# Performance work log

Hardware: AMD Instinct MI355X
Metric: run time of the kernel (lower is better)

The kernel has to match this reference:

```python
import jax, jax.numpy as jnp
import numpy as np

B, S, C, H = 1024, 254, 2, 1024
TIME_DIM = 64
HALF = TIME_DIM // 2
N_STEPS = 50


def time_embed(t):
    # t: [B] -> [B, 64] sinusoidal embedding, matching SinusoidalEmbedding(64)
    freqs = jnp.exp(jnp.arange(HALF, dtype=jnp.float32) * (-np.log(10000.0) / (HALF - 1)))
    ang = t[:, None] * freqs[None, :]  # [B, 32]
    return jnp.concatenate([jnp.sin(ang), jnp.cos(ang)], axis=-1)  # [B, 64]


def setup_inputs() -> dict:
    key = jax.random.key(0)
    ks = jax.random.split(key, 12)
    inp = {}
    inp["state"] = jax.random.normal(ks[0], (B, S), jnp.float32)
    inp["x0"] = jax.random.normal(ks[1], (B, C), jnp.float32)  # initial noise of sample()
    dims = [S + C + TIME_DIM, H, H, H, H, C]  # 320 -> 1024 x4 -> 2
    for i in range(5):
        kw, kb = jax.random.split(ks[2 + i])
        inp[f"W{i}"] = jax.random.normal(kw, (dims[i], dims[i + 1]), jnp.float32) * (1.0 / np.sqrt(dims[i]))
        inp[f"b{i}"] = jax.random.normal(kb, (dims[i + 1],), jnp.float32) * 0.01
    return inp


def reference(state, x0, W0, b0, W1, b1, W2, b2, W3, b3, W4, b4):
    dt = 1.0 / N_STEPS

    def velocity(x, t):
        temb = time_embed(t)
        h = jnp.concatenate([state, x, temb], axis=-1)  # [B, 320]
        h = jax.nn.silu(h @ W0 + b0)
        h = jax.nn.silu(h @ W1 + b1)
        h = jax.nn.silu(h @ W2 + b2)
        h = jax.nn.silu(h @ W3 + b3)
        return h @ W4 + b4  # [B, C]

    def step(x, i):
        t = jnp.full((state.shape[0],), i * dt, dtype=jnp.float32)
        return x + dt * velocity(x, t), None

    x, _ = jax.lax.scan(step, x0, jnp.arange(N_STEPS, dtype=jnp.float32))
    return x
```

## Files before the change

### kernel.cpp

```cpp
#include <hip/hip_runtime.h>


typedef __bf16 bf16x8 __attribute__((ext_vector_type(8)));
typedef float  f32x4  __attribute__((ext_vector_type(4)));
typedef unsigned short u16;
typedef u16 u16x8 __attribute__((ext_vector_type(8)));
typedef u16 u16x4 __attribute__((ext_vector_type(4)));

#define H 1024
#define BATCH 1024
#define SDIM 254
#define NSTEP 50
#define DT 0.02f
#define LDP 40

__device__ __forceinline__ u16 f2bf(float f) {
  unsigned int u = __float_as_uint(f);
  return (u16)((u + 0x7FFFu + ((u >> 16) & 1u)) >> 16);
}

__device__ __forceinline__ float silu(float v) {
  return v / (1.0f + __expf(-v));
}

__global__ void transpose_w(const float* __restrict__ A, const float* __restrict__ B,
                            const float* __restrict__ C, u16* __restrict__ TA,
                            u16* __restrict__ TB, u16* __restrict__ TC) {
  const float* W = (blockIdx.z == 0) ? A : (blockIdx.z == 1) ? B : C;
  u16* T = (blockIdx.z == 0) ? TA : (blockIdx.z == 1) ? TB : TC;
  __shared__ float tile[32][33];
  const int n0 = blockIdx.x * 32, k0 = blockIdx.y * 32;
  const int tx = threadIdx.x & 31, ty = threadIdx.x >> 5;
#pragma unroll
  for (int i = 0; i < 4; ++i)
    tile[ty + 8 * i][tx] = W[(k0 + ty + 8 * i) * H + n0 + tx];
  __syncthreads();
#pragma unroll
  for (int i = 0; i < 4; ++i)
    T[(size_t)(n0 + ty + 8 * i) * H + k0 + tx] = f2bf(tile[tx][ty + 8 * i]);
}

__global__ void base_gemm(const float* __restrict__ state, const float* __restrict__ W0,
                          const float* __restrict__ b0, float* __restrict__ base) {
  __shared__ float srow[SDIM];
  const int b = blockIdx.x, tid = threadIdx.x;
  if (tid < SDIM) srow[tid] = state[b * SDIM + tid];
  __syncthreads();
  const int n = tid * 4;
  float4 bv = *(const float4*)&b0[n];
  float a0 = bv.x, a1 = bv.y, a2 = bv.z, a3 = bv.w;
  for (int k = 0; k < SDIM; ++k) {
    float s = srow[k];
    float4 w = *(const float4*)&W0[k * H + n];
    a0 += s * w.x; a1 += s * w.y; a2 += s * w.z; a3 += s * w.w;
  }
  float4 r = {a0, a1, a2, a3};
  *(float4*)&base[(size_t)b * H + n] = r;
}

__global__ void tvec_kernel(const float* __restrict__ W0, float* __restrict__ tvec) {
  const int s = blockIdx.x;
  const int h = blockIdx.y * 256 + threadIdx.x;
  const float t = (float)s * DT;
  float acc = 0.0f;
#pragma unroll
  for (int j = 0; j < 32; ++j) {
    float fr = __expf((float)j * (-9.210340371976184f / 31.0f));
    float ang = t * fr;
    acc += __sinf(ang) * W0[(256 + j) * H + h] + __cosf(ang) * W0[(288 + j) * H + h];
  }
  tvec[s * H + h] = acc;
}

__global__ void init_kernel(const float* __restrict__ base, const float* __restrict__ tvec,
                            const float* __restrict__ x0, const float* __restrict__ W0,
                            u16* __restrict__ h0, float* __restrict__ xout) {
  const int b = blockIdx.x, tid = threadIdx.x;
  const float xa = x0[2 * b], xb = x0[2 * b + 1];
  if (tid == 0) { xout[2 * b] = xa; xout[2 * b + 1] = xb; }
  const int n = tid * 4;
  float4 bs = *(const float4*)&base[(size_t)b * H + n];
  float4 tv = *(const float4*)&tvec[n];
  float4 wa = *(const float4*)&W0[254 * H + n];
  float4 wb = *(const float4*)&W0[255 * H + n];
  u16x4 r;
  r[0] = f2bf(silu(bs.x + tv.x + xa * wa.x + xb * wb.x));
  r[1] = f2bf(silu(bs.y + tv.y + xa * wa.y + xb * wb.y));
  r[2] = f2bf(silu(bs.z + tv.z + xa * wa.z + xb * wb.z));
  r[3] = f2bf(silu(bs.w + tv.w + xa * wa.w + xb * wb.w));
  *(u16x4*)&h0[(size_t)b * H + n] = r;
}

__global__ __launch_bounds__(64) void gemm_mfma(const u16* __restrict__ A,
                                                const u16* __restrict__ BT,
                                                const float* __restrict__ bias,
                                                void* __restrict__ out, int out_bf16) {
  __shared__ u16 As[32 * LDP];
  __shared__ u16 Bs[32 * LDP];
  const int tid = threadIdx.x;
  const int bn = blockIdx.x, bm = blockIdx.y;
  const int lr = tid & 15, quad = tid >> 4;

  const int srow = tid >> 2;
  const int skc = (tid & 3) * 8;

  const u16* Ap = A + (size_t)(bm * 32 + srow) * H + skc;
  const u16* Bp = BT + (size_t)(bn * 32 + srow) * H + skc;

  f32x4 acc[2][2] = {};

  u16x8 ga0 = *(const u16x8*)(Ap);
  u16x8 ga1 = *(const u16x8*)(Ap + 16 * H);
  u16x8 gb0 = *(const u16x8*)(Bp);
  u16x8 gb1 = *(const u16x8*)(Bp + 16 * H);

  for (int kt = 0; kt < 32; ++kt) {
    *(u16x8*)&As[srow * LDP + skc] = ga0;
    *(u16x8*)&As[(srow + 16) * LDP + skc] = ga1;
    *(u16x8*)&Bs[srow * LDP + skc] = gb0;
    *(u16x8*)&Bs[(srow + 16) * LDP + skc] = gb1;
    if (kt < 31) {
      const int off = (kt + 1) * 32;
      ga0 = *(const u16x8*)(Ap + off);
      ga1 = *(const u16x8*)(Ap + 16 * H + off);
      gb0 = *(const u16x8*)(Bp + off);
      gb1 = *(const u16x8*)(Bp + 16 * H + off);
    }
    bf16x8 a0 = *(const bf16x8*)&As[lr * LDP + quad * 8];
    bf16x8 a1 = *(const bf16x8*)&As[(16 + lr) * LDP + quad * 8];
    bf16x8 b0 = *(const bf16x8*)&Bs[lr * LDP + quad * 8];
    bf16x8 b1 = *(const bf16x8*)&Bs[(16 + lr) * LDP + quad * 8];
    acc[0][0] = __builtin_amdgcn_mfma_f32_16x16x32_bf16(a0, b0, acc[0][0], 0, 0, 0);
    acc[0][1] = __builtin_amdgcn_mfma_f32_16x16x32_bf16(a0, b1, acc[0][1], 0, 0, 0);
    acc[1][0] = __builtin_amdgcn_mfma_f32_16x16x32_bf16(a1, b0, acc[1][0], 0, 0, 0);
    acc[1][1] = __builtin_amdgcn_mfma_f32_16x16x32_bf16(a1, b1, acc[1][1], 0, 0, 0);
  }

#pragma unroll
  for (int mt = 0; mt < 2; ++mt)
#pragma unroll
    for (int nt = 0; nt < 2; ++nt) {
      const int gm = bm * 32 + mt * 16 + quad * 4;
      const int gn = bn * 32 + nt * 16 + lr;
      const float bv = bias[gn];
      f32x4 v = acc[mt][nt];
#pragma unroll
      for (int r = 0; r < 4; ++r) {
        float x = silu(v[r] + bv);
        if (out_bf16) ((u16*)out)[(size_t)(gm + r) * H + gn] = f2bf(x);
        else          ((float*)out)[(size_t)(gm + r) * H + gn] = x;
      }
    }
}

__global__ void tail_kernel(const float* __restrict__ h3, const float* __restrict__ W4,
                            const float* __restrict__ b4, float* __restrict__ x,
                            const float* __restrict__ base, const float* __restrict__ tvec,
                            const float* __restrict__ W0, u16* __restrict__ h0, int s) {
  const int b = blockIdx.x, tid = threadIdx.x;
  float s0 = 0.0f, s1 = 0.0f;
  for (int h = tid; h < H; h += 256) {
    float v = h3[(size_t)b * H + h];
    s0 += v * W4[2 * h];
    s1 += v * W4[2 * h + 1];
  }
#pragma unroll
  for (int o = 32; o > 0; o >>= 1) {
    s0 += __shfl_down(s0, o);
    s1 += __shfl_down(s1, o);
  }
  __shared__ float red[8];
  __shared__ float xs[2];
  const int w = tid >> 6;
  if ((tid & 63) == 0) { red[w * 2] = s0; red[w * 2 + 1] = s1; }
  __syncthreads();
  if (tid == 0) {
    float v0 = red[0] + red[2] + red[4] + red[6] + b4[0];
    float v1 = red[1] + red[3] + red[5] + red[7] + b4[1];
    float xa = x[2 * b] + DT * v0;
    float xb = x[2 * b + 1] + DT * v1;
    x[2 * b] = xa; x[2 * b + 1] = xb;
    xs[0] = xa; xs[1] = xb;
  }
  __syncthreads();
  if (s < NSTEP - 1) {
    const float xa = xs[0], xb = xs[1];
    const int n = tid * 4;
    float4 bs = *(const float4*)&base[(size_t)b * H + n];
    float4 tv = *(const float4*)&tvec[(size_t)(s + 1) * H + n];
    float4 wa = *(const float4*)&W0[254 * H + n];
    float4 wb = *(const float4*)&W0[255 * H + n];
    u16x4 r;
    r[0] = f2bf(silu(bs.x + tv.x + xa * wa.x + xb * wb.x));
    r[1] = f2bf(silu(bs.y + tv.y + xa * wa.y + xb * wb.y));
    r[2] = f2bf(silu(bs.z + tv.z + xa * wa.z + xb * wb.z));
    r[3] = f2bf(silu(bs.w + tv.w + xa * wa.w + xb * wb.w));
    *(u16x4*)&h0[(size_t)b * H + n] = r;
  }
}

extern "C" void kernel_launch(void* const* d_in, const int* in_sizes, int n_in,
                              void* d_out, int out_size, void* d_ws, size_t ws_size,
                              hipStream_t stream) {
  const float* state = (const float*)d_in[0];
  const float* x0    = (const float*)d_in[1];
  const float* W0    = (const float*)d_in[2];
  const float* b0    = (const float*)d_in[3];
  const float* W1    = (const float*)d_in[4];
  const float* b1    = (const float*)d_in[5];
  const float* W2    = (const float*)d_in[6];
  const float* b2    = (const float*)d_in[7];
  const float* W3    = (const float*)d_in[8];
  const float* b3    = (const float*)d_in[9];
  const float* W4    = (const float*)d_in[10];
  const float* b4    = (const float*)d_in[11];
  float* xout = (float*)d_out;

  char* ws = (char*)d_ws;
  const size_t MB = 1024 * 1024;
  float* base = (float*)(ws + 0);
  float* h3f  = (float*)(ws + 4 * MB);
  float* tvec = (float*)(ws + 8 * MB);
  u16* w1t = (u16*)(ws + 8 * MB + 256 * 1024);
  u16* w2t = (u16*)(ws + 10 * MB + 256 * 1024);
  u16* w3t = (u16*)(ws + 12 * MB + 256 * 1024);
  u16* hA  = (u16*)(ws + 14 * MB + 256 * 1024);
  u16* hB  = (u16*)(ws + 16 * MB + 256 * 1024);
  u16* hC  = (u16*)(ws + 18 * MB + 256 * 1024);

  transpose_w<<<dim3(32, 32, 3), 256, 0, stream>>>(W1, W2, W3, w1t, w2t, w3t);
  base_gemm<<<BATCH, 256, 0, stream>>>(state, W0, b0, base);
  tvec_kernel<<<dim3(NSTEP, 4), 256, 0, stream>>>(W0, tvec);
  init_kernel<<<BATCH, 256, 0, stream>>>(base, tvec, x0, W0, hA, xout);

  for (int s = 0; s < NSTEP; ++s) {
    gemm_mfma<<<dim3(32, 32), 64, 0, stream>>>(hA, w1t, b1, hB, 1);
    gemm_mfma<<<dim3(32, 32), 64, 0, stream>>>(hB, w2t, b2, hC, 1);
    gemm_mfma<<<dim3(32, 32), 64, 0, stream>>>(hC, w3t, b3, h3f, 0);
    tail_kernel<<<BATCH, 256, 0, stream>>>(h3f, W4, b4, xout, base, tvec, W0, hA, s);
  }
}
```

Baseline: 1.837 ms.

## Load MFMA operands directly from global with 8-deep register prefetch, swizzle tiles

The GEMM kernel drops the shared-memory staging and loads bf16x8 fragments straight from global memory into registers, keeping eight k-tiles in flight as a rotating prefetch buffer. Block indices are remapped so groups of 8 M-tiles share an N-tile, which should improve L2 reuse. The fp32 state x W0 base GEMM is replaced by a bf16 transpose of W0, a bf16 padded copy of state, and the templated MFMA kernel. This removes LDS round-trips and barriers per k-step, at the cost of more registers and bf16 precision in the base projection.

```diff
diff --git a/kernel.cpp b/kernel.cpp
--- a/kernel.cpp
+++ b/kernel.cpp
@@ -4,7 +4,6 @@
 typedef __bf16 bf16x8 __attribute__((ext_vector_type(8)));
 typedef float  f32x4  __attribute__((ext_vector_type(4)));
 typedef unsigned short u16;
-typedef u16 u16x8 __attribute__((ext_vector_type(8)));
 typedef u16 u16x4 __attribute__((ext_vector_type(4)));
 
 #define H 1024
@@ -12,7 +11,6 @@
 #define SDIM 254
 #define NSTEP 50
 #define DT 0.02f
-#define LDP 40
 
 __device__ __forceinline__ u16 f2bf(float f) {
   unsigned int u = __float_as_uint(f);
@@ -40,22 +38,22 @@
     T[(size_t)(n0 + ty + 8 * i) * H + k0 + tx] = f2bf(tile[tx][ty + 8 * i]);
 }
 
-__global__ void base_gemm(const float* __restrict__ state, const float* __restrict__ W0,
-                          const float* __restrict__ b0, float* __restrict__ base) {
-  __shared__ float srow[SDIM];
-  const int b = blockIdx.x, tid = threadIdx.x;
-  if (tid < SDIM) srow[tid] = state[b * SDIM + tid];
-  __syncthreads();
-  const int n = tid * 4;
-  float4 bv = *(const float4*)&b0[n];
-  float a0 = bv.x, a1 = bv.y, a2 = bv.z, a3 = bv.w;
-  for (int k = 0; k < SDIM; ++k) {
-    float s = srow[k];
-    float4 w = *(const float4*)&W0[k * H + n];
-    a0 += s * w.x; a1 += s * w.y; a2 += s * w.z; a3 += s * w.w;
-  }
-  float4 r = {a0, a1, a2, a3};
-  *(float4*)&base[(size_t)b * H + n] = r;
+__global__ void transpose_w0(const float* __restrict__ W0, u16* __restrict__ T) {
+  __shared__ float tile[32][33];
+  const int n0 = blockIdx.x * 32, k0 = blockIdx.y * 32;
+  const int tx = threadIdx.x & 31, ty = threadIdx.x >> 5;
+#pragma unroll
+  for (int i = 0; i < 4; ++i)
+    tile[ty + 8 * i][tx] = W0[(k0 + ty + 8 * i) * H + n0 + tx];
+  __syncthreads();
+#pragma unroll
+  for (int i = 0; i < 4; ++i)
+    T[(size_t)(n0 + ty + 8 * i) * 256 + k0 + tx] = f2bf(tile[tx][ty + 8 * i]);
+}
+
+__global__ void prep_state(const float* __restrict__ state, u16* __restrict__ sb) {
+  const int row = blockIdx.x, col = threadIdx.x;
+  sb[row * 256 + col] = (col < SDIM) ? f2bf(state[row * SDIM + col]) : (u16)0;
 }
 
 __global__ void tvec_kernel(const float* __restrict__ W0, float* __restrict__ tvec) {
@@ -91,49 +89,45 @@
   *(u16x4*)&h0[(size_t)b * H + n] = r;
 }
 
+template <int KTILES, int MODE>
 __global__ __launch_bounds__(64) void gemm_mfma(const u16* __restrict__ A,
                                                 const u16* __restrict__ BT,
                                                 const float* __restrict__ bias,
-                                                void* __restrict__ out, int out_bf16) {
-  __shared__ u16 As[32 * LDP];
-  __shared__ u16 Bs[32 * LDP];
+                                                void* __restrict__ out) {
   const int tid = threadIdx.x;
-  const int bn = blockIdx.x, bm = blockIdx.y;
   const int lr = tid & 15, quad = tid >> 4;
-
-  const int srow = tid >> 2;
-  const int skc = (tid & 3) * 8;
-
-  const u16* Ap = A + (size_t)(bm * 32 + srow) * H + skc;
-  const u16* Bp = BT + (size_t)(bn * 32 + srow) * H + skc;
-
+  const int lin = blockIdx.x + 32 * blockIdx.y;
+  const int bm = (lin & 7) | ((lin >> 8) << 3);
+  const int bn = (lin >> 3) & 31;
+  const int K = KTILES * 32;
+
+  const bf16x8* Ap0 = (const bf16x8*)(A + (size_t)(bm * 32 + lr) * K + quad * 8);
+  const bf16x8* Ap1 = (const bf16x8*)(A + (size_t)(bm * 32 + 16 + lr) * K + quad * 8);
+  const bf16x8* Bp0 = (const bf16x8*)(BT + (size_t)(bn * 32 + lr) * K + quad * 8);
+  const bf16x8* Bp1 = (const bf16x8*)(BT + (size_t)(bn * 32 + 16 + lr) * K + quad * 8);
   f32x4 acc[2][2] = {};
-
-  u16x8 ga0 = *(const u16x8*)(Ap);
-  u16x8 ga1 = *(const u16x8*)(Ap + 16 * H);
-  u16x8 gb0 = *(const u16x8*)(Bp);
-  u16x8 gb1 = *(const u16x8*)(Bp + 16 * H);
-
-  for (int kt = 0; kt < 32; ++kt) {
-    *(u16x8*)&As[srow * LDP + skc] = ga0;
-    *(u16x8*)&As[(srow + 16) * LDP + skc] = ga1;
-    *(u16x8*)&Bs[srow * LDP + skc] = gb0;
-    *(u16x8*)&Bs[(srow + 16) * LDP + skc] = gb1;
-    if (kt < 31) {
-      const int off = (kt + 1) * 32;
-      ga0 = *(const u16x8*)(Ap + off);
-      ga1 = *(const u16x8*)(Ap + 16 * H + off);
-      gb0 = *(const u16x8*)(Bp + off);
-      gb1 = *(const u16x8*)(Bp + 16 * H + off);
+  bf16x8 pa0[8], pa1[8], pb0[8], pb1[8];
+#pragma unroll
+  for (int d = 0; d < 8 && d < KTILES; ++d) {
+    pa0[d] = Ap0[d * 4];
+    pa1[d] = Ap1[d * 4];
+    pb0[d] = Bp0[d * 4];
+    pb1[d] = Bp1[d * 4];
+  }
+#pragma unroll
+  for (int kt = 0; kt < KTILES; ++kt) {
+    const int s = kt & 7;
+    acc[0][0] = __builtin_amdgcn_mfma_f32_16x16x32_bf16(pa0[s], pb0[s], acc[0][0], 0, 0, 0);
+    acc[0][1] = __builtin_amdgcn_mfma_f32_16x16x32_bf16(pa0[s], pb1[s], acc[0][1], 0, 0, 0);
+    acc[1][0] = __builtin_amdgcn_mfma_f32_16x16x32_bf16(pa1[s], pb0[s], acc[1][0], 0, 0, 0);
+    acc[1][1] = __builtin_amdgcn_mfma_f32_16x16x32_bf16(pa1[s], pb1[s], acc[1][1], 0, 0, 0);
+    if (kt + 8 < KTILES) {
+      const int off = (kt + 8) * 4;
+      pa0[s] = Ap0[off];
+      pa1[s] = Ap1[off];
+      pb0[s] = Bp0[off];
+      pb1[s] = Bp1[off];
     }
-    bf16x8 a0 = *(const bf16x8*)&As[lr * LDP + quad * 8];
-    bf16x8 a1 = *(const bf16x8*)&As[(16 + lr) * LDP + quad * 8];
-    bf16x8 b0 = *(const bf16x8*)&Bs[lr * LDP + quad * 8];
-    bf16x8 b1 = *(const bf16x8*)&Bs[(16 + lr) * LDP + quad * 8];
-    acc[0][0] = __builtin_amdgcn_mfma_f32_16x16x32_bf16(a0, b0, acc[0][0], 0, 0, 0);
-    acc[0][1] = __builtin_amdgcn_mfma_f32_16x16x32_bf16(a0, b1, acc[0][1], 0, 0, 0);
-    acc[1][0] = __builtin_amdgcn_mfma_f32_16x16x32_bf16(a1, b0, acc[1][0], 0, 0, 0);
-    acc[1][1] = __builtin_amdgcn_mfma_f32_16x16x32_bf16(a1, b1, acc[1][1], 0, 0, 0);
   }
 
 #pragma unroll
@@ -146,9 +140,10 @@
       f32x4 v = acc[mt][nt];
 #pragma unroll
       for (int r = 0; r < 4; ++r) {
-        float x = silu(v[r] + bv);
-        if (out_bf16) ((u16*)out)[(size_t)(gm + r) * H + gn] = f2bf(x);
-        else          ((float*)out)[(size_t)(gm + r) * H + gn] = x;
+        float x = v[r] + bv;
+        if (MODE != 2) x = silu(x);
+        if (MODE == 0) ((u16*)out)[(size_t)(gm + r) * H + gn] = f2bf(x);
+        else           ((float*)out)[(size_t)(gm + r) * H + gn] = x;
       }
     }
 }
@@ -227,16 +222,20 @@
   u16* hA  = (u16*)(ws + 14 * MB + 256 * 1024);
   u16* hB  = (u16*)(ws + 16 * MB + 256 * 1024);
   u16* hC  = (u16*)(ws + 18 * MB + 256 * 1024);
+  u16* w0t = (u16*)(ws + 20 * MB + 256 * 1024);
+  u16* stb = (u16*)(ws + 21 * MB);
 
   transpose_w<<<dim3(32, 32, 3), 256, 0, stream>>>(W1, W2, W3, w1t, w2t, w3t);
-  base_gemm<<<BATCH, 256, 0, stream>>>(state, W0, b0, base);
+  transpose_w0<<<dim3(32, 8), 256, 0, stream>>>(W0, w0t);
+  prep_state<<<BATCH, 256, 0, stream>>>(state, stb);
+  gemm_mfma<8, 2><<<dim3(32, 32), 64, 0, stream>>>(stb, w0t, b0, base);
   tvec_kernel<<<dim3(NSTEP, 4), 256, 0, stream>>>(W0, tvec);
   init_kernel<<<BATCH, 256, 0, stream>>>(base, tvec, x0, W0, hA, xout);
 
   for (int s = 0; s < NSTEP; ++s) {
-    gemm_mfma<<<dim3(32, 32), 64, 0, stream>>>(hA, w1t, b1, hB, 1);
-    gemm_mfma<<<dim3(32, 32), 64, 0, stream>>>(hB, w2t, b2, hC, 1);
-    gemm_mfma<<<dim3(32, 32), 64, 0, stream>>>(hC, w3t, b3, h3f, 0);
+    gemm_mfma<32, 0><<<dim3(32, 32), 64, 0, stream>>>(hA, w1t, b1, hB);
+    gemm_mfma<32, 0><<<dim3(32, 32), 64, 0, stream>>>(hB, w2t, b2, hC);
+    gemm_mfma<32, 1><<<dim3(32, 32), 64, 0, stream>>>(hC, w3t, b3, h3f);
     tail_kernel<<<BATCH, 256, 0, stream>>>(h3f, W4, b4, xout, base, tvec, W0, hA, s);
   }
 }
```

Result: slower. 3.038 ms (+65.4%).
